# Kernel optimization log

Hardware: AMD Instinct MI355X
Metric: run time of the kernel (lower is better)

## Reference

```python
import jax, jax.numpy as jnp
import numpy as np

WIN = 16
SIGMA = 1.5
DATA_RANGE = 255.0
C1 = (0.01 * DATA_RANGE) ** 2
C2 = (0.03 * DATA_RANGE) ** 2
MSE_W = 0.7
SSIM_W = 0.3


def _gauss_window(channels):
    # 16x16 gaussian window, sigma=1.5, normalized to sum 1
    coords = np.arange(WIN, dtype=np.float32) - (WIN - 1) / 2.0
    g = np.exp(-(coords ** 2) / (2.0 * SIGMA ** 2))
    g = g / g.sum()
    w2d = np.outer(g, g)  # [16,16]
    w = np.broadcast_to(w2d, (channels, 1, WIN, WIN)).copy()
    return jnp.asarray(w)


def _depthwise_conv(x, w):
    # x: [B,C,H,W], w: [C,1,k,k] depthwise, VALID padding
    return jax.lax.conv_general_dilated(
        x, w, window_strides=(1, 1), padding='VALID',
        dimension_numbers=('NCHW', 'OIHW', 'NCHW'),
        feature_group_count=x.shape[1])


def _ssim(img1, img2):
    # images assumed in [0,255] (PIL-equivalent range)
    C = img1.shape[1]
    w = _gauss_window(C).astype(img1.dtype)
    mu1 = _depthwise_conv(img1, w)
    mu2 = _depthwise_conv(img2, w)
    mu1_sq = mu1 * mu1
    mu2_sq = mu2 * mu2
    mu12 = mu1 * mu2
    sigma1_sq = _depthwise_conv(img1 * img1, w) - mu1_sq
    sigma2_sq = _depthwise_conv(img2 * img2, w) - mu2_sq
    sigma12 = _depthwise_conv(img1 * img2, w) - mu12
    ssim_map = ((2.0 * mu12 + C1) * (2.0 * sigma12 + C2)) / (
        (mu1_sq + mu2_sq + C1) * (sigma1_sq + sigma2_sq + C2))
    # per-sample mean, then mean over batch (matches batch_ssim loop + .mean())
    return jnp.mean(ssim_map, axis=(1, 2, 3)).mean()


def setup_inputs() -> dict:
    key = jax.random.key(0)
    k1, k2 = jax.random.split(key)
    shape = (32, 3, 512, 512)
    output = jax.random.uniform(k1, shape, dtype=jnp.float32)
    target = jax.random.uniform(k2, shape, dtype=jnp.float32)
    return {'output': output, 'target': target}


def reference(output, target):
    mse_loss = jnp.mean((output - target) ** 2)
    # to_pil_image scales [0,1] float tensors to [0,255] uint8; SSIM computed
    # in 0-255 range with data_range=255
    ssim_val = _ssim(output * 255.0, target * 255.0)
    ssim_loss = 1.0 - ssim_val
    return mse_loss * MSE_W + ssim_loss * SSIM_W
```

## Files before the change

kernel.cpp:

```cpp
#include <hip/hip_runtime.h>
#include <math.h>
#include <string.h>

typedef __attribute__((ext_vector_type(8))) short bf16x8;
typedef __attribute__((ext_vector_type(4))) float f32x4;

namespace {
constexpr int TOUT = 32;
constexpr int IMG  = 512;
constexpr int HALO = 15;
constexpr int OUTW = IMG - HALO;
constexpr int NBLK = 16 * 16 * 96;

struct WinPk { unsigned w[8]; };

__device__ __forceinline__ unsigned prm(unsigned hi, unsigned lo) {
    return __builtin_amdgcn_perm(hi, lo, 0x07060302u);
}
}

template <bool TWO_STAGE>
__global__ __launch_bounds__(256, 8)
void ssim_mse_kernel(const float* __restrict__ img1,
                     const float* __restrict__ img2,
                     WinPk wpk,
                     double2* __restrict__ partial,
                     double*  __restrict__ accum)
{
    __shared__ unsigned short S[4][48][48];
    __shared__ unsigned short gt[64];
    __shared__ float red[2][4];

    const int tid = threadIdx.x;
    const int ox0 = blockIdx.x * TOUT;
    const int oy0 = blockIdx.y * TOUT;
    const size_t plane_off = (size_t)blockIdx.z * (IMG * IMG);
    const float* __restrict__ p1 = img1 + plane_off;
    const float* __restrict__ p2 = img2 + plane_off;

    float mse_local = 0.0f, ssim_local = 0.0f;

    if (tid < 16) gt[tid] = 0;
    else if (tid >= 32 && tid < 64) gt[tid] = 0;
    else if (tid == 16) {
        #pragma unroll
        for (int k = 0; k < 8; ++k)
            *(unsigned*)&gt[16 + 2 * k] = wpk.w[k];
    }

    for (int it = tid; it < 288; it += 256) {
        const int r   = (int)((unsigned)it / 6u);
        const int cs8 = it - 6 * r;
        const int c0  = 8 * cs8;
        if (r == 47) {
            const uint4 z = make_uint4(0u, 0u, 0u, 0u);
            *(uint4*)&S[0][47][c0] = z;
            *(uint4*)&S[1][47][c0] = z;
            *(uint4*)&S[2][47][c0] = z;
            *(uint4*)&S[3][47][c0] = z;
        } else {
            const int gy  = oy0 + r;
            const int gyc = gy < IMG ? gy : IMG - 1;
            const float* __restrict__ pa = p1 + (size_t)gyc * IMG;
            const float* __restrict__ pb = p2 + (size_t)gyc * IMG;
            float Af[8], Bf[8];
            if (ox0 + c0 + 8 <= IMG) {
                const float4 va0 = *(const float4*)(pa + ox0 + c0);
                const float4 va1 = *(const float4*)(pa + ox0 + c0 + 4);
                const float4 vb0 = *(const float4*)(pb + ox0 + c0);
                const float4 vb1 = *(const float4*)(pb + ox0 + c0 + 4);
                Af[0] = va0.x; Af[1] = va0.y; Af[2] = va0.z; Af[3] = va0.w;
                Af[4] = va1.x; Af[5] = va1.y; Af[6] = va1.z; Af[7] = va1.w;
                Bf[0] = vb0.x; Bf[1] = vb0.y; Bf[2] = vb0.z; Bf[3] = vb0.w;
                Bf[4] = vb1.x; Bf[5] = vb1.y; Bf[6] = vb1.z; Bf[7] = vb1.w;
            } else {
                #pragma unroll
                for (int j = 0; j < 8; ++j) {
                    int gx = ox0 + c0 + j; gx = gx < IMG ? gx : IMG - 1;
                    Af[j] = pa[gx]; Bf[j] = pb[gx];
                }
            }
            if (r < TOUT && cs8 < 4) {
                #pragma unroll
                for (int j = 0; j < 8; ++j) {
                    const float d = Af[j] - Bf[j];
                    mse_local = fmaf(d, d, mse_local);
                }
            }
            unsigned wA[4], wB[4], wQ[4], wX[4];
            #pragma unroll
            for (int h = 0; h < 4; ++h) {
                const unsigned a0 = __float_as_uint(Af[2*h])   + 0x8000u;
                const unsigned a1 = __float_as_uint(Af[2*h+1]) + 0x8000u;
                const unsigned b0 = __float_as_uint(Bf[2*h])   + 0x8000u;
                const unsigned b1 = __float_as_uint(Bf[2*h+1]) + 0x8000u;
                const float ar0 = __uint_as_float(a0 & 0xFFFF0000u);
                const float ar1 = __uint_as_float(a1 & 0xFFFF0000u);
                const float br0 = __uint_as_float(b0 & 0xFFFF0000u);
                const float br1 = __uint_as_float(b1 & 0xFFFF0000u);
                const unsigned q0 = __float_as_uint(fmaf(ar0, ar0, br0 * br0)) + 0x8000u;
                const unsigned q1 = __float_as_uint(fmaf(ar1, ar1, br1 * br1)) + 0x8000u;
                const unsigned x0 = __float_as_uint(ar0 * br0) + 0x8000u;
                const unsigned x1 = __float_as_uint(ar1 * br1) + 0x8000u;
                wA[h] = prm(a1, a0); wB[h] = prm(b1, b0);
                wQ[h] = prm(q1, q0); wX[h] = prm(x1, x0);
            }
            if (cs8 == 5) {
                wA[3] &= 0xFFFFu; wB[3] &= 0xFFFFu;
                wQ[3] &= 0xFFFFu; wX[3] &= 0xFFFFu;
            }
            uint4 vA, vB, vQ, vX;
            vA.x = wA[0]; vA.y = wA[1]; vA.z = wA[2]; vA.w = wA[3];
            vB.x = wB[0]; vB.y = wB[1]; vB.z = wB[2]; vB.w = wB[3];
            vQ.x = wQ[0]; vQ.y = wQ[1]; vQ.z = wQ[2]; vQ.w = wQ[3];
            vX.x = wX[0]; vX.y = wX[1]; vX.z = wX[2]; vX.w = wX[3];
            *(uint4*)&S[0][r][c0] = vA;
            *(uint4*)&S[1][r][c0] = vB;
            *(uint4*)&S[2][r][c0] = vQ;
            *(uint4*)&S[3][r][c0] = vX;
        }
    }
    __syncthreads();

    const int m15 = tid & 15;
    const int q4  = (tid >> 4) & 3;
    const int wid = tid >> 6;

    bf16x8 wf;
    {
        const int base = q4 * 8 - m15 + 16;
        #pragma unroll
        for (int j = 0; j < 8; ++j)
            wf[j] = (short)gt[base + j];
    }

    {
        auto hstep = [&](const bf16x8 af, const int Mt, const int Nt) {
            f32x4 c = {0.f, 0.f, 0.f, 0.f};
            c = __builtin_amdgcn_mfma_f32_16x16x32_bf16(af, wf, c, 0, 0, 0);
            const unsigned lo = prm(__float_as_uint(c[1]) + 0x8000u,
                                    __float_as_uint(c[0]) + 0x8000u);
            const unsigned hi = prm(__float_as_uint(c[3]) + 0x8000u,
                                    __float_as_uint(c[2]) + 0x8000u);
            uint2 wv; wv.x = lo; wv.y = hi;
            *(uint2*)&S[wid][Nt * 16 + m15][Mt * 16 + q4 * 4] = wv;
        };
        const bf16x8 a00 = *(const bf16x8*)&S[wid][     m15][     q4 * 8];
        const bf16x8 a01 = *(const bf16x8*)&S[wid][     m15][16 + q4 * 8];
        const bf16x8 a10 = *(const bf16x8*)&S[wid][16 + m15][     q4 * 8];
        const bf16x8 a11 = *(const bf16x8*)&S[wid][16 + m15][16 + q4 * 8];
        hstep(a00, 0, 0);
        hstep(a01, 0, 1);
        hstep(a10, 1, 0);
        hstep(a11, 1, 1);
        const bf16x8 a20 = *(const bf16x8*)&S[wid][32 + m15][     q4 * 8];
        const bf16x8 a21 = *(const bf16x8*)&S[wid][32 + m15][16 + q4 * 8];
        hstep(a20, 2, 0);
        hstep(a21, 2, 1);
    }
    __syncthreads();

    {
        const int Rt = wid >> 1, Ct = wid & 1;
        const int ko = Rt * 16 + q4 * 8;
        const f32x4 z = {0.f, 0.f, 0.f, 0.f};
        const bf16x8 f0 = *(const bf16x8*)&S[0][Ct * 16 + m15][ko];
        const bf16x8 f1 = *(const bf16x8*)&S[1][Ct * 16 + m15][ko];
        const bf16x8 f2 = *(const bf16x8*)&S[2][Ct * 16 + m15][ko];
        const bf16x8 f3 = *(const bf16x8*)&S[3][Ct * 16 + m15][ko];
        const f32x4 M1 = __builtin_amdgcn_mfma_f32_16x16x32_bf16(wf, f0, z, 0, 0, 0);
        const f32x4 M2 = __builtin_amdgcn_mfma_f32_16x16x32_bf16(wf, f1, z, 0, 0, 0);
        const f32x4 Qm = __builtin_amdgcn_mfma_f32_16x16x32_bf16(wf, f2, z, 0, 0, 0);
        const f32x4 Xm = __builtin_amdgcn_mfma_f32_16x16x32_bf16(wf, f3, z, 0, 0, 0);

        const float C1u = 1.0e-4f;
        const float C2u = 9.0e-4f;
        const int ocol  = ox0 + Ct * 16 + m15;
        const int orow0 = oy0 + Rt * 16 + q4 * 4;
        #pragma unroll
        for (int g = 0; g < 4; ++g) {
            const float mu1  = M1[g], mu2 = M2[g];
            const float mu12 = mu1 * mu2;
            const float musq = fmaf(mu1, mu1, mu2 * mu2);
            const float sgq  = Qm[g] - musq;
            const float sg12 = Xm[g] - mu12;
            const float num  = fmaf(2.0f, mu12, C1u) * fmaf(2.0f, sg12, C2u);
            const float den  = (musq + C1u) * (sgq + C2u);
            const float val  = num * __builtin_amdgcn_rcpf(den);
            if (ocol < OUTW && (orow0 + g) < OUTW) ssim_local += val;
        }
    }

    #pragma unroll
    for (int off = 32; off > 0; off >>= 1) {
        mse_local  += __shfl_down(mse_local,  off, 64);
        ssim_local += __shfl_down(ssim_local, off, 64);
    }
    if ((tid & 63) == 0) { red[0][wid] = mse_local; red[1][wid] = ssim_local; }
    __syncthreads();
    if (tid == 0) {
        const double m = (double)red[0][0] + (double)red[0][1]
                       + (double)red[0][2] + (double)red[0][3];
        const double s = (double)red[1][0] + (double)red[1][1]
                       + (double)red[1][2] + (double)red[1][3];
        if (TWO_STAGE) {
            const int bid = (int)blockIdx.x
                          + 16 * ((int)blockIdx.y + 16 * (int)blockIdx.z);
            partial[bid] = make_double2(m, s);
        } else {
            atomicAdd(&accum[0], m);
            atomicAdd(&accum[1], s);
        }
    }
}

__global__ __launch_bounds__(1024) void reduce_kernel(
    const double2* __restrict__ partial,
    float* __restrict__ out)
{
    __shared__ double sm[16], ss[16];
    const int tid = threadIdx.x;
    double m = 0.0, s = 0.0;
    #pragma unroll
    for (int k = 0; k < 24; ++k) {
        const double2 p = partial[tid + 1024 * k];
        m += p.x; s += p.y;
    }
    #pragma unroll
    for (int off = 32; off > 0; off >>= 1) {
        m += __shfl_down(m, off, 64);
        s += __shfl_down(s, off, 64);
    }
    if ((tid & 63) == 0) { sm[tid >> 6] = m; ss[tid >> 6] = s; }
    __syncthreads();
    if (tid == 0) {
        double M = 0.0, S = 0.0;
        #pragma unroll
        for (int w = 0; w < 16; ++w) { M += sm[w]; S += ss[w]; }
        const double mse  = M / 25165824.0;
        const double ssim = S / 23712864.0;
        out[0] = (float)(0.7 * mse + 0.3 * (1.0 - ssim));
    }
}

__global__ void finalize_kernel(const double* __restrict__ accum,
                                float* __restrict__ out)
{
    const double mse  = accum[0] / 25165824.0;
    const double ssim = accum[1] / 23712864.0;
    out[0] = (float)(0.7 * mse + 0.3 * (1.0 - ssim));
}

extern "C" void kernel_launch(void* const* d_in, const int* in_sizes, int n_in,
                              void* d_out, int out_size, void* d_ws, size_t ws_size,
                              hipStream_t stream) {
    const float* img1 = (const float*)d_in[0];
    const float* img2 = (const float*)d_in[1];
    float* out = (float*)d_out;

    WinPk wpk;
    {
        double g[16], s = 0.0;
        for (int i = 0; i < 16; ++i) {
            const double c = (double)i - 7.5;
            g[i] = exp(-(c * c) / 4.5);
            s += g[i];
        }
        unsigned short h[16];
        for (int i = 0; i < 16; ++i) {
            const float gf = (float)(g[i] / s);
            unsigned u;
            memcpy(&u, &gf, 4);
            u += 0x7FFFu + ((u >> 16) & 1u);
            h[i] = (unsigned short)(u >> 16);
        }
        for (int k = 0; k < 8; ++k)
            wpk.w[k] = (unsigned)h[2 * k] | ((unsigned)h[2 * k + 1] << 16);
    }

    dim3 grid(16, 16, 96);
    if (ws_size >= (size_t)NBLK * sizeof(double2)) {
        double2* partial = (double2*)d_ws;
        ssim_mse_kernel<true><<<grid, dim3(256), 0, stream>>>(
            img1, img2, wpk, partial, nullptr);
        reduce_kernel<<<1, dim3(1024), 0, stream>>>(partial, out);
    } else {
        double* accum = (double*)d_ws;
        hipMemsetAsync(d_ws, 0, 2 * sizeof(double), stream);
        ssim_mse_kernel<false><<<grid, dim3(256), 0, stream>>>(
            img1, img2, wpk, nullptr, accum);
        finalize_kernel<<<1, 1, 0, stream>>>(accum, out);
    }
}
```

Before: 232.3 us.

## Widen SSIM tile to 64x32 outputs with 512-thread blocks and padded LDS

Each block now computes a 64-wide by 32-tall output tile with 512 threads, so the 15-pixel horizontal halo is shared by more outputs and less redundant global loading and bf16 conversion happens per output. The LDS layout becomes flat, with padded strides (88 for input rows, 56 for the transposed intermediate). The horizontal-pass results are held in registers across an extra barrier before being written back transposed, since the wider tile reuses the same planes. The grid and reduce loop are halved to match. In exchange, blocks use more LDS and threads, which may lower residency per CU.

Result: faster. 222.4 us (-4.3%).

```diff
diff --git a/kernel.cpp b/kernel.cpp
--- a/kernel.cpp
+++ b/kernel.cpp
@@ -6,11 +6,14 @@
 typedef __attribute__((ext_vector_type(4))) float f32x4;
 
 namespace {
-constexpr int TOUT = 32;
 constexpr int IMG  = 512;
 constexpr int HALO = 15;
 constexpr int OUTW = IMG - HALO;
-constexpr int NBLK = 16 * 16 * 96;
+constexpr int NBLK = 8 * 16 * 96;
+
+constexpr int SSTR = 88;
+constexpr int PLN  = 48 * SSTR;
+constexpr int HSTR = 56;
 
 struct WinPk { unsigned w[8]; };
 
@@ -20,20 +23,20 @@
 }
 
 template <bool TWO_STAGE>
-__global__ __launch_bounds__(256, 8)
+__global__ __launch_bounds__(512, 8)
 void ssim_mse_kernel(const float* __restrict__ img1,
                      const float* __restrict__ img2,
                      WinPk wpk,
                      double2* __restrict__ partial,
                      double*  __restrict__ accum)
 {
-    __shared__ unsigned short S[4][48][48];
+    __shared__ unsigned short S[4 * PLN];
     __shared__ unsigned short gt[64];
-    __shared__ float red[2][4];
+    __shared__ float red[2][8];
 
     const int tid = threadIdx.x;
-    const int ox0 = blockIdx.x * TOUT;
-    const int oy0 = blockIdx.y * TOUT;
+    const int ox0 = blockIdx.x * 64;
+    const int oy0 = blockIdx.y * 32;
     const size_t plane_off = (size_t)blockIdx.z * (IMG * IMG);
     const float* __restrict__ p1 = img1 + plane_off;
     const float* __restrict__ p2 = img2 + plane_off;
@@ -48,16 +51,17 @@
             *(unsigned*)&gt[16 + 2 * k] = wpk.w[k];
     }
 
-    for (int it = tid; it < 288; it += 256) {
-        const int r   = (int)((unsigned)it / 6u);
-        const int cs8 = it - 6 * r;
+    if (tid < 480) {
+        const int r   = (int)((unsigned)tid / 10u);
+        const int cs8 = tid - 10 * r;
         const int c0  = 8 * cs8;
+        const int sb  = r * SSTR + c0;
         if (r == 47) {
             const uint4 z = make_uint4(0u, 0u, 0u, 0u);
-            *(uint4*)&S[0][47][c0] = z;
-            *(uint4*)&S[1][47][c0] = z;
-            *(uint4*)&S[2][47][c0] = z;
-            *(uint4*)&S[3][47][c0] = z;
+            *(uint4*)&S[0 * PLN + sb] = z;
+            *(uint4*)&S[1 * PLN + sb] = z;
+            *(uint4*)&S[2 * PLN + sb] = z;
+            *(uint4*)&S[3 * PLN + sb] = z;
         } else {
             const int gy  = oy0 + r;
             const int gyc = gy < IMG ? gy : IMG - 1;
@@ -80,7 +84,7 @@
                     Af[j] = pa[gx]; Bf[j] = pb[gx];
                 }
             }
-            if (r < TOUT && cs8 < 4) {
+            if (r < 32 && cs8 < 8) {
                 #pragma unroll
                 for (int j = 0; j < 8; ++j) {
                     const float d = Af[j] - Bf[j];
@@ -105,7 +109,7 @@
                 wA[h] = prm(a1, a0); wB[h] = prm(b1, b0);
                 wQ[h] = prm(q1, q0); wX[h] = prm(x1, x0);
             }
-            if (cs8 == 5) {
+            if (cs8 == 9) {
                 wA[3] &= 0xFFFFu; wB[3] &= 0xFFFFu;
                 wQ[3] &= 0xFFFFu; wX[3] &= 0xFFFFu;
             }
@@ -114,10 +118,10 @@
             vB.x = wB[0]; vB.y = wB[1]; vB.z = wB[2]; vB.w = wB[3];
             vQ.x = wQ[0]; vQ.y = wQ[1]; vQ.z = wQ[2]; vQ.w = wQ[3];
             vX.x = wX[0]; vX.y = wX[1]; vX.z = wX[2]; vX.w = wX[3];
-            *(uint4*)&S[0][r][c0] = vA;
-            *(uint4*)&S[1][r][c0] = vB;
-            *(uint4*)&S[2][r][c0] = vQ;
-            *(uint4*)&S[3][r][c0] = vX;
+            *(uint4*)&S[0 * PLN + sb] = vA;
+            *(uint4*)&S[1 * PLN + sb] = vB;
+            *(uint4*)&S[2 * PLN + sb] = vQ;
+            *(uint4*)&S[3 * PLN + sb] = vX;
         }
     }
     __syncthreads();
@@ -135,39 +139,49 @@
     }
 
     {
-        auto hstep = [&](const bf16x8 af, const int Mt, const int Nt) {
-            f32x4 c = {0.f, 0.f, 0.f, 0.f};
-            c = __builtin_amdgcn_mfma_f32_16x16x32_bf16(af, wf, c, 0, 0, 0);
-            const unsigned lo = prm(__float_as_uint(c[1]) + 0x8000u,
-                                    __float_as_uint(c[0]) + 0x8000u);
-            const unsigned hi = prm(__float_as_uint(c[3]) + 0x8000u,
-                                    __float_as_uint(c[2]) + 0x8000u);
-            uint2 wv; wv.x = lo; wv.y = hi;
-            *(uint2*)&S[wid][Nt * 16 + m15][Mt * 16 + q4 * 4] = wv;
-        };
-        const bf16x8 a00 = *(const bf16x8*)&S[wid][     m15][     q4 * 8];
-        const bf16x8 a01 = *(const bf16x8*)&S[wid][     m15][16 + q4 * 8];
-        const bf16x8 a10 = *(const bf16x8*)&S[wid][16 + m15][     q4 * 8];
-        const bf16x8 a11 = *(const bf16x8*)&S[wid][16 + m15][16 + q4 * 8];
-        hstep(a00, 0, 0);
-        hstep(a01, 0, 1);
-        hstep(a10, 1, 0);
-        hstep(a11, 1, 1);
-        const bf16x8 a20 = *(const bf16x8*)&S[wid][32 + m15][     q4 * 8];
-        const bf16x8 a21 = *(const bf16x8*)&S[wid][32 + m15][16 + q4 * 8];
-        hstep(a20, 2, 0);
-        hstep(a21, 2, 1);
+        const int s  = wid & 3;
+        const int nh = wid >> 2;
+        uint2 hw[6];
+        #pragma unroll
+        for (int NtL = 0; NtL < 2; ++NtL) {
+            const int Nt = 2 * nh + NtL;
+            #pragma unroll
+            for (int Mt = 0; Mt < 3; ++Mt) {
+                const bf16x8 af = *(const bf16x8*)
+                    &S[s * PLN + (Mt * 16 + m15) * SSTR + Nt * 16 + q4 * 8];
+                f32x4 c = {0.f, 0.f, 0.f, 0.f};
+                c = __builtin_amdgcn_mfma_f32_16x16x32_bf16(af, wf, c, 0, 0, 0);
+                const unsigned lo = prm(__float_as_uint(c[1]) + 0x8000u,
+                                        __float_as_uint(c[0]) + 0x8000u);
+                const unsigned hi = prm(__float_as_uint(c[3]) + 0x8000u,
+                                        __float_as_uint(c[2]) + 0x8000u);
+                uint2 wv; wv.x = lo; wv.y = hi;
+                hw[NtL * 3 + Mt] = wv;
+            }
+        }
+        __syncthreads();
+        #pragma unroll
+        for (int NtL = 0; NtL < 2; ++NtL) {
+            const int Nt = 2 * nh + NtL;
+            #pragma unroll
+            for (int Mt = 0; Mt < 3; ++Mt) {
+                const int oc = Nt * 16 + m15;
+                const int hr = Mt * 16 + q4 * 4;
+                *(uint2*)&S[s * PLN + oc * HSTR + hr] = hw[NtL * 3 + Mt];
+            }
+        }
     }
     __syncthreads();
 
     {
-        const int Rt = wid >> 1, Ct = wid & 1;
+        const int Rt = wid >> 2, Ct = wid & 3;
         const int ko = Rt * 16 + q4 * 8;
+        const int ob = (Ct * 16 + m15) * HSTR + ko;
         const f32x4 z = {0.f, 0.f, 0.f, 0.f};
-        const bf16x8 f0 = *(const bf16x8*)&S[0][Ct * 16 + m15][ko];
-        const bf16x8 f1 = *(const bf16x8*)&S[1][Ct * 16 + m15][ko];
-        const bf16x8 f2 = *(const bf16x8*)&S[2][Ct * 16 + m15][ko];
-        const bf16x8 f3 = *(const bf16x8*)&S[3][Ct * 16 + m15][ko];
+        const bf16x8 f0 = *(const bf16x8*)&S[0 * PLN + ob];
+        const bf16x8 f1 = *(const bf16x8*)&S[1 * PLN + ob];
+        const bf16x8 f2 = *(const bf16x8*)&S[2 * PLN + ob];
+        const bf16x8 f3 = *(const bf16x8*)&S[3 * PLN + ob];
         const f32x4 M1 = __builtin_amdgcn_mfma_f32_16x16x32_bf16(wf, f0, z, 0, 0, 0);
         const f32x4 M2 = __builtin_amdgcn_mfma_f32_16x16x32_bf16(wf, f1, z, 0, 0, 0);
         const f32x4 Qm = __builtin_amdgcn_mfma_f32_16x16x32_bf16(wf, f2, z, 0, 0, 0);
@@ -199,13 +213,15 @@
     if ((tid & 63) == 0) { red[0][wid] = mse_local; red[1][wid] = ssim_local; }
     __syncthreads();
     if (tid == 0) {
-        const double m = (double)red[0][0] + (double)red[0][1]
-                       + (double)red[0][2] + (double)red[0][3];
-        const double s = (double)red[1][0] + (double)red[1][1]
-                       + (double)red[1][2] + (double)red[1][3];
+        double m = 0.0, s = 0.0;
+        #pragma unroll
+        for (int w = 0; w < 8; ++w) {
+            m += (double)red[0][w];
+            s += (double)red[1][w];
+        }
         if (TWO_STAGE) {
             const int bid = (int)blockIdx.x
-                          + 16 * ((int)blockIdx.y + 16 * (int)blockIdx.z);
+                          + 8 * ((int)blockIdx.y + 16 * (int)blockIdx.z);
             partial[bid] = make_double2(m, s);
         } else {
             atomicAdd(&accum[0], m);
@@ -222,7 +238,7 @@
     const int tid = threadIdx.x;
     double m = 0.0, s = 0.0;
     #pragma unroll
-    for (int k = 0; k < 24; ++k) {
+    for (int k = 0; k < 12; ++k) {
         const double2 p = partial[tid + 1024 * k];
         m += p.x; s += p.y;
     }
@@ -278,16 +294,16 @@
             wpk.w[k] = (unsigned)h[2 * k] | ((unsigned)h[2 * k + 1] << 16);
     }
 
-    dim3 grid(16, 16, 96);
+    dim3 grid(8, 16, 96);
     if (ws_size >= (size_t)NBLK * sizeof(double2)) {
         double2* partial = (double2*)d_ws;
-        ssim_mse_kernel<true><<<grid, dim3(256), 0, stream>>>(
+        ssim_mse_kernel<true><<<grid, dim3(512), 0, stream>>>(
             img1, img2, wpk, partial, nullptr);
         reduce_kernel<<<1, dim3(1024), 0, stream>>>(partial, out);
     } else {
         double* accum = (double*)d_ws;
         hipMemsetAsync(d_ws, 0, 2 * sizeof(double), stream);
-        ssim_mse_kernel<false><<<grid, dim3(256), 0, stream>>>(
+        ssim_mse_kernel<false><<<grid, dim3(512), 0, stream>>>(
             img1, img2, wpk, nullptr, accum);
         finalize_kernel<<<1, 1, 0, stream>>>(accum, out);
     }
```
